# Kernel tuning notes

Measured on AMD Instinct MI355X. Metric: run time of the kernel, lower is better.

## Reference

```python
import jax, jax.numpy as jnp
import numpy as np

D = 256      # input_size == output_size
H = 8        # head_count
DH = D // H  # dim per head


def setup_inputs() -> dict:
    key = jax.random.key(0)
    ks = jax.random.split(key, 11)
    s = 1.0 / np.sqrt(D)
    inp = {
        "x": jax.random.normal(ks[0], (4, 2048, D), dtype=jnp.float32),
        "Wq": jax.random.normal(ks[1], (D, D), dtype=jnp.float32) * s,
        "bq": jnp.zeros((D,), jnp.float32),
        "Wk": jax.random.normal(ks[2], (D, D), dtype=jnp.float32) * s,
        "bk": jnp.zeros((D,), jnp.float32),
        "Wv": jax.random.normal(ks[3], (D, D), dtype=jnp.float32) * s,
        "bv": jnp.zeros((D,), jnp.float32),
        "Wo": jax.random.normal(ks[4], (D, D), dtype=jnp.float32) * s,
        "bo": jnp.zeros((D,), jnp.float32),
        "Wc": jax.random.normal(ks[5], (D, D), dtype=jnp.float32) * s,
        "bc": jnp.zeros((D,), jnp.float32),
    }
    return inp


def _split_heads(t):
    b, n, _ = t.shape
    return t.reshape(b, n, H, DH).transpose(0, 2, 1, 3)  # b h n dh


def reference(x, Wq, bq, Wk, bk, Wv, bv, Wo, bo, Wc, bc):
    # Multi-head self-attention over all nodes (complete graph)
    q = _split_heads(x @ Wq + bq)
    k = _split_heads(x @ Wk + bk)
    v = _split_heads(x @ Wv + bv)
    scale = 1.0 / jnp.sqrt(jnp.asarray(DH, x.dtype))
    scores = jnp.einsum("bhqd,bhkd->bhqk", q * scale, k)
    attn = jax.nn.softmax(scores, axis=-1)  # attn dropout = identity (eval)
    ctx = jnp.einsum("bhqk,bhkd->bhqd", attn, v)
    b, _, n, _ = ctx.shape
    ctx = ctx.transpose(0, 2, 1, 3).reshape(b, n, D)
    ctx = ctx @ Wo + bo  # MHA output projection
    # linear_context + dropout (identity in eval) + residual
    out = x + (ctx @ Wc + bc)
    return out
```

## Files before the change

kernel.cpp:

```cpp
#include <hip/hip_runtime.h>

#define DMODEL 256
#define HEADS 8
#define DHEAD 32
#define NSEQ 2048
#define BATCH 4
#define MTOT (BATCH*NSEQ)

typedef __bf16 bf16x8 __attribute__((ext_vector_type(8)));
typedef float f32x4 __attribute__((ext_vector_type(4)));

#define CSH 32.649321103346387f
#define EXPC 16252.0f

__device__ __forceinline__ unsigned short f2bf(float f) {
    union { float f; unsigned int u; } v; v.f = f;
    unsigned int u = v.u;
    unsigned int r = u + 0x7FFFu + ((u >> 16) & 1u);
    return (unsigned short)(r >> 16);
}

__device__ __forceinline__ unsigned pkbf(float a, float b) {
    union { __bf16 h[2]; unsigned u; } t;
    t.h[0] = (__bf16)a; t.h[1] = (__bf16)b;
    return t.u;
}

__device__ __forceinline__ unsigned pkexp(float a, float b) {
    int ia = (int)a;
    int ib = (int)b;
    return __builtin_amdgcn_perm((unsigned)ib, (unsigned)ia, 0x05040100u);
}

__device__ __forceinline__ f32x4 mfma16(bf16x8 a, bf16x8 b, f32x4 c) {
    return __builtin_amdgcn_mfma_f32_16x16x32_bf16(a, b, c, 0, 0, 0);
}

#define GLD16(g, l) __builtin_amdgcn_global_load_lds( \
    (const __attribute__((address_space(1))) unsigned int*)(g), \
    (__attribute__((address_space(3))) unsigned int*)(l), 16, 0, 0)

__global__ __launch_bounds__(256) void prep_kernel(
    const float* __restrict__ x,
    const float* __restrict__ Wq, const float* __restrict__ Wk,
    const float* __restrict__ Wv, const float* __restrict__ Wo,
    const float* __restrict__ Wc,
    const float* __restrict__ bq, const float* __restrict__ bk,
    const float* __restrict__ bv, const float* __restrict__ bo,
    const float* __restrict__ bc,
    unsigned short* __restrict__ xbf,
    unsigned short* __restrict__ Wt,
    float* __restrict__ bcat,
    unsigned short* __restrict__ Woct,
    float* __restrict__ bocf)
{
    const int tid = threadIdx.x;
    if (blockIdx.x < 257) {
        int k = blockIdx.x;
        int n = tid;
        const float* arow = (k < 256) ? (Wo + k * 256) : bo;
        float a0 = 0.f, a1 = 0.f, a2 = 0.f, a3 = 0.f;
#pragma unroll 4
        for (int j = 0; j < 256; j += 4) {
            a0 = fmaf(arow[j],     Wc[j * 256 + n],       a0);
            a1 = fmaf(arow[j + 1], Wc[(j + 1) * 256 + n], a1);
            a2 = fmaf(arow[j + 2], Wc[(j + 2) * 256 + n], a2);
            a3 = fmaf(arow[j + 3], Wc[(j + 3) * 256 + n], a3);
        }
        float acc = (a0 + a1) + (a2 + a3);
        if (k < 256) Woct[n * 256 + k] = f2bf(acc);
        else         bocf[n] = acc + bc[n];
        return;
    }
    if (blockIdx.x < 2305) {
        int idx = (blockIdx.x - 257) * 256 + tid;
        float4 v = reinterpret_cast<const float4*>(x)[idx];
        ushort4 o;
        o.x = f2bf(v.x); o.y = f2bf(v.y); o.z = f2bf(v.z); o.w = f2bf(v.w);
        reinterpret_cast<ushort4*>(xbf)[idx] = o;
        return;
    }
    if (blockIdx.x < 2385) {
        __shared__ unsigned short Lt[64 * 72];
        const int bb = blockIdx.x - 2305;
        const int wid = tid >> 6, lane = tid & 63;
        const int n0 = (bb >> 2) * 64, k0 = (bb & 3) * 64;
        const float* Wsrc; int col0;
        if (n0 < 256)       { Wsrc = Wq; col0 = n0; }
        else if (n0 < 512)  { Wsrc = Wk; col0 = n0 - 256; }
        else if (n0 < 768)  { Wsrc = Wv; col0 = n0 - 512; }
        else if (n0 < 1024) { Wsrc = Wo; col0 = n0 - 768; }
        else                { Wsrc = Wc; col0 = n0 - 1024; }
#pragma unroll
        for (int r = 0; r < 16; ++r) {
            int k = k0 + wid * 16 + r;
            Lt[lane * 72 + wid * 16 + r] = f2bf(Wsrc[k * 256 + col0 + lane]);
        }
        __syncthreads();
#pragma unroll
        for (int c = tid; c < 512; c += 256) {
            int row = c >> 3, seg = c & 7;
            *reinterpret_cast<bf16x8*>(Wt + (n0 + row) * 256 + k0 + seg * 8) =
                *reinterpret_cast<const bf16x8*>(Lt + row * 72 + seg * 8);
        }
        return;
    }
    int t = (blockIdx.x - 2385) * 256 + tid;
    if (t < 1280) {
        float v;
        if (t < 256)       v = bq[t];
        else if (t < 512)  v = bk[t - 256];
        else if (t < 768)  v = bv[t - 512];
        else if (t < 1024) v = bo[t - 768];
        else               v = bc[t - 1024];
        bcat[t] = v;
    }
}

__global__ __launch_bounds__(256) void gemm_qkv(
    const unsigned short* __restrict__ A,
    const unsigned short* __restrict__ Wt,
    const float* __restrict__ bias,
    unsigned short* __restrict__ outQ,
    unsigned short* __restrict__ outK,
    unsigned short* __restrict__ outVt)
{
    __shared__ __align__(16) unsigned short Bl[64 * 256];
    const int tid = threadIdx.x;
    const int wid = tid >> 6;
    const int lane = tid & 63;
    const int lo = lane & 15, hi = lane >> 4;
    const int m0 = blockIdx.x * 128 + wid * 32;
    const int n0 = blockIdx.y * 64;

#pragma unroll
    for (int j = 0; j < 8; ++j) {
        int chunkbase = (j * 4 + wid) * 64;
        int chunk = chunkbase + lane;
        int row = chunk >> 5, Jp = chunk & 31;
        int J = (Jp & 24) | ((Jp ^ row) & 7);
        GLD16(Wt + (n0 + row) * 256 + J * 8, Bl + chunkbase * 8);
    }
    asm volatile("s_waitcnt vmcnt(0)" ::: "memory");
    __syncthreads();

    const unsigned short* arow0 = A + (m0 + lo) * 256 + hi * 8;
    f32x4 acc[2][4] = {};
#pragma unroll
    for (int s = 0; s < 8; ++s) {
        bf16x8 a0 = *reinterpret_cast<const bf16x8*>(arow0 + s * 32);
        bf16x8 a1 = *reinterpret_cast<const bf16x8*>(arow0 + 16 * 256 + s * 32);
        int Jp = ((s >> 1) << 3) | ((((s & 1) << 2) + hi) ^ (lo & 7));
#pragma unroll
        for (int n = 0; n < 4; ++n) {
            bf16x8 b = *reinterpret_cast<const bf16x8*>(
                Bl + (n * 16 + lo) * 256 + Jp * 8);
            acc[0][n] = mfma16(a0, b, acc[0][n]);
            acc[1][n] = mfma16(a1, b, acc[1][n]);
        }
    }

    const int type = blockIdx.y >> 2;
    const int m0b = blockIdx.x * 128;
    unsigned short* Lb = Bl;
    __syncthreads();
    if (type < 2) {
#pragma unroll
        for (int mf = 0; mf < 2; ++mf)
#pragma unroll
        for (int n = 0; n < 4; ++n) {
            float bs = bias[n0 + n * 16 + lo];
#pragma unroll
            for (int i = 0; i < 4; ++i) {
                float val = acc[mf][n][i] + bs;
                if (type == 0) val *= CSH;
                Lb[(wid * 32 + mf * 16 + hi * 4 + i) * 72 + n * 16 + lo] = f2bf(val);
            }
        }
    } else {
#pragma unroll
        for (int mf = 0; mf < 2; ++mf)
#pragma unroll
        for (int n = 0; n < 4; ++n) {
            float bs = bias[n0 + n * 16 + lo];
            uint2 pk;
            pk.x = pkbf(acc[mf][n][0] + bs, acc[mf][n][1] + bs);
            pk.y = pkbf(acc[mf][n][2] + bs, acc[mf][n][3] + bs);
            *reinterpret_cast<uint2*>(
                Lb + (n * 16 + lo) * 136 + wid * 32 + mf * 16 + hi * 4) = pk;
        }
    }
    __syncthreads();
    if (type < 2) {
        unsigned short* outP = (type == 0) ? outQ : outK;
#pragma unroll
        for (int r = 0; r < 4; ++r) {
            int cid = r * 256 + tid;
            int m_l = cid >> 3, seg = cid & 7;
            bf16x8 chunk = *reinterpret_cast<const bf16x8*>(Lb + m_l * 72 + seg * 8);
            int m = m0b + m_l, gc = n0 + seg * 8;
            int b = m >> 11, nn = m & 2047, hh = (gc >> 5) & 7, dh = gc & 31;
            *reinterpret_cast<bf16x8*>(
                outP + (((b * 8) + hh) * 2048 + nn) * 32 + dh) = chunk;
        }
    } else {
#pragma unroll
        for (int r = 0; r < 4; ++r) {
            int cid = r * 256 + tid;
            int gcl = cid >> 4, seg = cid & 15;
            const unsigned short* src = Lb + gcl * 136 + seg * 8;
            uint2 lo4 = *reinterpret_cast<const uint2*>(src);
            uint2 hi4 = *reinterpret_cast<const uint2*>(src + 4);
            int gc = n0 + gcl, m = m0b + seg * 8;
            int b = m >> 11, nn = m & 2047, hh = (gc >> 5) & 7, dh = gc & 31;
            int pos0 = (nn & ~63) | (nn & 32) | ((nn & 8) << 1) | ((nn & 16) >> 2);
            unsigned short* dst = outVt + (((b * 8) + hh) * 32 + dh) * 2048;
            *reinterpret_cast<uint2*>(dst + pos0)     = lo4;
            *reinterpret_cast<uint2*>(dst + pos0 + 8) = hi4;
        }
    }
}

__global__ __launch_bounds__(256, 4) void attn_kernel(
    const unsigned short* __restrict__ Q,
    const unsigned short* __restrict__ K,
    const unsigned short* __restrict__ Vt,
    unsigned short* __restrict__ ctx)
{
    __shared__ __align__(16) char smem[32768];

    const int tid = threadIdx.x;
    const int wid = tid >> 6;
    const int lane = tid & 63;
    const int lo = lane & 15, hi = lane >> 4;
    const int qsub = wid & 1;
    const int half = wid >> 1;

    const int bid = blockIdx.x;
    const int bh = ((bid >> 7) << 3) | (bid & 7);
    const int qt = (bid >> 3) & 15;
    const int q0 = qt * 128 + qsub * 64;

    const unsigned short* Qb = Q + bh * (NSEQ * 32);
    const unsigned short* Kh0 = K + bh * (NSEQ * 32) + (half * 1024) * 32;
    const unsigned short* Vh0 = Vt + bh * (32 * NSEQ) + half * 1024;

    bf16x8 qf[4];
#pragma unroll
    for (int g = 0; g < 4; ++g)
        qf[g] = *reinterpret_cast<const bf16x8*>(
            Qb + (q0 + g * 16 + lo) * 32 + hi * 8);

    const int lt2 = tid & 127;
    const int cA = lt2, cB = lt2 + 128;
    const unsigned short* kA0 = Kh0 + (2 * (cA >> 3) + ((cA >> 2) & 1)) * 32
                                    + ((cA & 3) ^ ((cA >> 3) & 3)) * 8;
    const unsigned short* kA1 = Kh0 + (2 * (cB >> 3) + ((cB >> 2) & 1)) * 32
                                    + ((cB & 3) ^ ((cB >> 3) & 3)) * 8;
    const unsigned short* vA0 = Vh0 + (cA >> 3) * NSEQ
                                    + ((cA & 7) ^ ((cA >> 3) & 7)) * 8;
    const unsigned short* vA1 = Vh0 + (cB >> 3) * NSEQ
                                    + ((cB & 7) ^ ((cB >> 3) & 7)) * 8;
    char* kd0 = smem + half * 8192 + lt2 * 16;
    char* kd1 = kd0 + 2048;
    char* vd0 = smem + 16384 + half * 8192 + lt2 * 16;
    char* vd1 = vd0 + 2048;

    f32x4 o0[4] = {}, o1[4] = {}, od[4] = {};
    const f32x4 ec = {EXPC, EXPC, EXPC, EXPC};
    const int prs = lo & 7;
    const int kxor = (hi ^ ((lo >> 1) & 3)) * 8;

    union { unsigned u[4]; bf16x8 v; } ones;
    ones.u[0] = 0x3F803F80u; ones.u[1] = 0x3F803F80u;
    ones.u[2] = 0x3F803F80u; ones.u[3] = 0x3F803F80u;

#define STAGE_T(tt, buf) do { \
    GLD16(kA0 + (tt) * 2048, kd0 + (buf) * 4096); \
    GLD16(kA1 + (tt) * 2048, kd1 + (buf) * 4096); \
    GLD16(vA0 + (tt) * 64,   vd0 + (buf) * 4096); \
    GLD16(vA1 + (tt) * 64,   vd1 + (buf) * 4096); \
} while (0)

    STAGE_T(0, 0);
    asm volatile("s_waitcnt vmcnt(0)" ::: "memory");
    __builtin_amdgcn_s_barrier();
    __builtin_amdgcn_sched_barrier(0);

    int cur = 0;
    for (int t = 0; t < 16; ++t) {
        if (t < 15) STAGE_T(t + 1, cur ^ 1);
        const unsigned short* Kh =
            (const unsigned short*)(smem + half * 8192 + cur * 4096);
        const unsigned short* Vh =
            (const unsigned short*)(smem + 16384 + half * 8192 + cur * 4096);

        __builtin_amdgcn_s_setprio(1);
        f32x4 s[4][4];
#pragma unroll
        for (int c = 0; c < 4; ++c) {
            bf16x8 kf = *reinterpret_cast<const bf16x8*>(
                Kh + (c * 16 + lo) * 32 + kxor);
#pragma unroll
            for (int g = 0; g < 4; ++g)
                s[g][c] = mfma16(kf, qf[g], ec);
        }
#pragma unroll
        for (int kk = 0; kk < 2; ++kk) {
            int sw = ((4 * kk + hi) ^ prs) * 8;
            bf16x8 a0 = *reinterpret_cast<const bf16x8*>(Vh + lo * 64 + sw);
            bf16x8 a1 = *reinterpret_cast<const bf16x8*>(Vh + (16 + lo) * 64 + sw);
#pragma unroll
            for (int g = 0; g < 4; ++g) {
                const f32x4 s0 = s[g][2 * kk], s1 = s[g][2 * kk + 1];
                union { unsigned u[4]; bf16x8 v; } pb;
                pb.u[0] = pkexp(s0[0], s0[1]);
                pb.u[1] = pkexp(s0[2], s0[3]);
                pb.u[2] = pkexp(s1[0], s1[1]);
                pb.u[3] = pkexp(s1[2], s1[3]);
                o0[g] = mfma16(a0, pb.v, o0[g]);
                o1[g] = mfma16(a1, pb.v, o1[g]);
                od[g] = mfma16(ones.v, pb.v, od[g]);
            }
        }
        __builtin_amdgcn_s_setprio(0);

        if (t < 15) {
            asm volatile("s_waitcnt vmcnt(0)" ::: "memory");
            __builtin_amdgcn_s_barrier();
            __builtin_amdgcn_sched_barrier(0);
            cur ^= 1;
        }
    }

    float* comb = (float*)smem;
    const int cidx = (qsub * 64 + lane) * 48;
    __syncthreads();
    if (half) {
#pragma unroll
        for (int g = 0; g < 4; ++g) {
            *reinterpret_cast<f32x4*>(comb + cidx + g * 12)     = o0[g];
            *reinterpret_cast<f32x4*>(comb + cidx + g * 12 + 4) = o1[g];
            comb[cidx + g * 12 + 8] = od[g][0];
        }
    }
    __syncthreads();
    if (!half) {
        const int b = bh >> 3, h = bh & 7;
#pragma unroll
        for (int g = 0; g < 4; ++g) {
            f32x4 p0 = *reinterpret_cast<const f32x4*>(comb + cidx + g * 12);
            f32x4 p1 = *reinterpret_cast<const f32x4*>(comb + cidx + g * 12 + 4);
            float inv = 1.0f / (od[g][0] + comb[cidx + g * 12 + 8]);
            f32x4 r0 = o0[g] + p0, r1 = o1[g] + p1;
            unsigned short* dst = ctx
                + (size_t)((b * 2048 + q0 + g * 16 + lo)) * 256 + h * 32;
            ushort4 w0, w1;
            w0.x = f2bf(r0[0] * inv); w0.y = f2bf(r0[1] * inv);
            w0.z = f2bf(r0[2] * inv); w0.w = f2bf(r0[3] * inv);
            w1.x = f2bf(r1[0] * inv); w1.y = f2bf(r1[1] * inv);
            w1.z = f2bf(r1[2] * inv); w1.w = f2bf(r1[3] * inv);
            *reinterpret_cast<ushort4*>(dst + hi * 4)      = w0;
            *reinterpret_cast<ushort4*>(dst + 16 + hi * 4) = w1;
        }
    }
#undef STAGE_T
}

__global__ __launch_bounds__(256) void gemm_ctx(
    const unsigned short* __restrict__ A,
    const unsigned short* __restrict__ Wt,
    const float* __restrict__ boc,
    const float* __restrict__ xres,
    float* __restrict__ outF)
{
    __shared__ __align__(16) unsigned short Bl[64 * 256];
    const int tid = threadIdx.x;
    const int wid = tid >> 6;
    const int lane = tid & 63;
    const int lo = lane & 15, hi = lane >> 4;
    const int m0 = blockIdx.x * 128 + wid * 32;
    const int n0 = blockIdx.y * 64;

#pragma unroll
    for (int j = 0; j < 8; ++j) {
        int chunkbase = (j * 4 + wid) * 64;
        int chunk = chunkbase + lane;
        int row = chunk >> 5, Jp = chunk & 31;
        int J = (Jp & 24) | ((Jp ^ row) & 7);
        GLD16(Wt + (n0 + row) * 256 + J * 8, Bl + chunkbase * 8);
    }
    asm volatile("s_waitcnt vmcnt(0)" ::: "memory");
    __syncthreads();

    const unsigned short* arow0 = A + (m0 + lo) * 256 + hi * 8;
    f32x4 acc[2][4] = {};
#pragma unroll
    for (int s = 0; s < 8; ++s) {
        bf16x8 a0 = *reinterpret_cast<const bf16x8*>(arow0 + s * 32);
        bf16x8 a1 = *reinterpret_cast<const bf16x8*>(arow0 + 16 * 256 + s * 32);
        int Jp = ((s >> 1) << 3) | ((((s & 1) << 2) + hi) ^ (lo & 7));
#pragma unroll
        for (int n = 0; n < 4; ++n) {
            bf16x8 b = *reinterpret_cast<const bf16x8*>(
                Bl + (n * 16 + lo) * 256 + Jp * 8);
            acc[0][n] = mfma16(a0, b, acc[0][n]);
            acc[1][n] = mfma16(a1, b, acc[1][n]);
        }
    }
#pragma unroll
    for (int mf = 0; mf < 2; ++mf) {
        const int row_base = m0 + mf * 16 + hi * 4;
#pragma unroll
        for (int n = 0; n < 4; ++n) {
            int gc = n0 + n * 16 + lo;
            float bs = boc[gc];
#pragma unroll
            for (int i = 0; i < 4; ++i)
                outF[(row_base + i) * 256 + gc] =
                    xres[(row_base + i) * 256 + gc] + acc[mf][n][i] + bs;
        }
    }
}

extern "C" void kernel_launch(void* const* d_in, const int* in_sizes, int n_in,
                              void* d_out, int out_size, void* d_ws, size_t ws_size,
                              hipStream_t stream) {
    const float* x  = (const float*)d_in[0];
    const float* Wq = (const float*)d_in[1];
    const float* bq = (const float*)d_in[2];
    const float* Wk = (const float*)d_in[3];
    const float* bk = (const float*)d_in[4];
    const float* Wv = (const float*)d_in[5];
    const float* bv = (const float*)d_in[6];
    const float* Wo = (const float*)d_in[7];
    const float* bo = (const float*)d_in[8];
    const float* Wc = (const float*)d_in[9];
    const float* bc = (const float*)d_in[10];
    float* out = (float*)d_out;

    char* p = (char*)d_ws;
    unsigned short* xbf  = (unsigned short*)p;  p += (size_t)MTOT * DMODEL * 2;
    unsigned short* Wt   = (unsigned short*)p;  p += (size_t)1280 * 256 * 2;
    float* bcat          = (float*)p;           p += (size_t)1280 * 4;
    unsigned short* Qw   = (unsigned short*)p;  p += (size_t)32 * 2048 * 32 * 2;
    unsigned short* Kw   = (unsigned short*)p;  p += (size_t)32 * 2048 * 32 * 2;
    unsigned short* Vtw  = (unsigned short*)p;  p += (size_t)32 * 32 * 2048 * 2;
    unsigned short* ctx  = (unsigned short*)p;  p += (size_t)MTOT * DMODEL * 2;
    unsigned short* Woct = (unsigned short*)p;  p += (size_t)256 * 256 * 2;
    float* bocf          = (float*)p;           p += (size_t)256 * 4;

    prep_kernel<<<2390, 256, 0, stream>>>(x, Wq, Wk, Wv, Wo, Wc,
                                          bq, bk, bv, bo, bc,
                                          xbf, Wt, bcat, Woct, bocf);
    gemm_qkv<<<dim3(64, 12), 256, 0, stream>>>(xbf, Wt, bcat, Qw, Kw, Vtw);
    attn_kernel<<<512, 256, 0, stream>>>(Qw, Kw, Vtw, ctx);
    gemm_ctx<<<dim3(64, 4), 256, 0, stream>>>(ctx, Woct, bocf, x, out);
}
```

Measured before the change: 61.18 us.

## Give each wave private K/V LDS buffers and drop per-tile block barriers

Each wave now stages its own copy of the K/V tiles into a private 16KB LDS region, so the per-iteration workgroup barriers are removed and waves proceed independently. This eliminates barrier stalls between waves, but pairs of waves sharing the same key half now load the same data twice. LDS use doubles to 64KB, and launch bounds drop to 2 blocks per CU, reducing occupancy.

New measurement: 52.29 us. 1.17x faster.

```diff
diff --git a/kernel.cpp b/kernel.cpp
--- a/kernel.cpp
+++ b/kernel.cpp
@@ -221,13 +221,13 @@
     }
 }
 
-__global__ __launch_bounds__(256, 4) void attn_kernel(
+__global__ __launch_bounds__(256, 2) void attn_kernel(
     const unsigned short* __restrict__ Q,
     const unsigned short* __restrict__ K,
     const unsigned short* __restrict__ Vt,
     unsigned short* __restrict__ ctx)
 {
-    __shared__ __align__(16) char smem[32768];
+    __shared__ __align__(16) char smem[65536];
 
     const int tid = threadIdx.x;
     const int wid = tid >> 6;
@@ -251,20 +251,18 @@
         qf[g] = *reinterpret_cast<const bf16x8*>(
             Qb + (q0 + g * 16 + lo) * 32 + hi * 8);
 
-    const int lt2 = tid & 127;
-    const int cA = lt2, cB = lt2 + 128;
-    const unsigned short* kA0 = Kh0 + (2 * (cA >> 3) + ((cA >> 2) & 1)) * 32
-                                    + ((cA & 3) ^ ((cA >> 3) & 3)) * 8;
-    const unsigned short* kA1 = Kh0 + (2 * (cB >> 3) + ((cB >> 2) & 1)) * 32
-                                    + ((cB & 3) ^ ((cB >> 3) & 3)) * 8;
-    const unsigned short* vA0 = Vh0 + (cA >> 3) * NSEQ
-                                    + ((cA & 7) ^ ((cA >> 3) & 7)) * 8;
-    const unsigned short* vA1 = Vh0 + (cB >> 3) * NSEQ
-                                    + ((cB & 7) ^ ((cB >> 3) & 7)) * 8;
-    char* kd0 = smem + half * 8192 + lt2 * 16;
-    char* kd1 = kd0 + 2048;
-    char* vd0 = smem + 16384 + half * 8192 + lt2 * 16;
-    char* vd1 = vd0 + 2048;
+    int ko0, ko1, ko2, ko3, vo0, vo1, vo2, vo3;
+    {
+        int c0 = lane, c1 = 64 + lane, c2 = 128 + lane, c3 = 192 + lane;
+#define KOFF(c) ((2 * ((c) >> 3) + (((c) & 7) >> 2)) * 32 + ((((c) & 3) ^ (((c) >> 3) & 3)) * 8))
+#define VOFF(c) (((c) >> 3) * NSEQ + ((((c) & 7) ^ (((c) >> 3) & 7)) * 8))
+        ko0 = KOFF(c0); ko1 = KOFF(c1); ko2 = KOFF(c2); ko3 = KOFF(c3);
+        vo0 = VOFF(c0); vo1 = VOFF(c1); vo2 = VOFF(c2); vo3 = VOFF(c3);
+#undef KOFF
+#undef VOFF
+    }
+    char* wb = smem + wid * 16384;
+    const int lb = lane * 16;
 
     f32x4 o0[4] = {}, o1[4] = {}, od[4] = {};
     const f32x4 ec = {EXPC, EXPC, EXPC, EXPC};
@@ -276,24 +274,29 @@
     ones.u[2] = 0x3F803F80u; ones.u[3] = 0x3F803F80u;
 
 #define STAGE_T(tt, buf) do { \
-    GLD16(kA0 + (tt) * 2048, kd0 + (buf) * 4096); \
-    GLD16(kA1 + (tt) * 2048, kd1 + (buf) * 4096); \
-    GLD16(vA0 + (tt) * 64,   vd0 + (buf) * 4096); \
-    GLD16(vA1 + (tt) * 64,   vd1 + (buf) * 4096); \
+    const unsigned short* kb_ = Kh0 + (tt) * 2048; \
+    const unsigned short* vb_ = Vh0 + (tt) * 64; \
+    char* kd_ = wb + (buf) * 8192 + lb; \
+    char* vd_ = wb + (buf) * 8192 + 4096 + lb; \
+    GLD16(kb_ + ko0, kd_);        \
+    GLD16(kb_ + ko1, kd_ + 1024); \
+    GLD16(kb_ + ko2, kd_ + 2048); \
+    GLD16(kb_ + ko3, kd_ + 3072); \
+    GLD16(vb_ + vo0, vd_);        \
+    GLD16(vb_ + vo1, vd_ + 1024); \
+    GLD16(vb_ + vo2, vd_ + 2048); \
+    GLD16(vb_ + vo3, vd_ + 3072); \
 } while (0)
 
     STAGE_T(0, 0);
     asm volatile("s_waitcnt vmcnt(0)" ::: "memory");
-    __builtin_amdgcn_s_barrier();
     __builtin_amdgcn_sched_barrier(0);
 
     int cur = 0;
     for (int t = 0; t < 16; ++t) {
         if (t < 15) STAGE_T(t + 1, cur ^ 1);
-        const unsigned short* Kh =
-            (const unsigned short*)(smem + half * 8192 + cur * 4096);
-        const unsigned short* Vh =
-            (const unsigned short*)(smem + 16384 + half * 8192 + cur * 4096);
+        const unsigned short* Kh = (const unsigned short*)(wb + cur * 8192);
+        const unsigned short* Vh = (const unsigned short*)(wb + cur * 8192 + 4096);
 
         __builtin_amdgcn_s_setprio(1);
         f32x4 s[4][4];
@@ -327,7 +330,6 @@
 
         if (t < 15) {
             asm volatile("s_waitcnt vmcnt(0)" ::: "memory");
-            __builtin_amdgcn_s_barrier();
             __builtin_amdgcn_sched_barrier(0);
             cur ^= 1;
         }
```
